# Kernel tuning notes

Measured on AMD Instinct MI355X. Metric: run time of the kernel, lower is better.

## Reference

```python
import jax, jax.numpy as jnp
import numpy as np
import math

NH, NKV, HD = 8, 1, 128
SOFTCAP = 30.0
ROPE_BASE = 500000.0


def _rope_tables(T, hd, base):
    half = hd // 2
    inv_freq = 1.0 / (base ** (np.arange(half, dtype=np.float32) / half))
    t = np.arange(T, dtype=np.float32)
    ang = np.outer(t, inv_freq)  # [T, half]
    return jnp.asarray(np.cos(ang)), jnp.asarray(np.sin(ang))


def apply_rope(x, cos, sin):
    # x: [B, T, H, hd]; cos/sin: [T, hd//2]
    half = x.shape[-1] // 2
    x1, x2 = x[..., :half], x[..., half:]
    T = x.shape[1]
    c = cos[:T][None, :, None, :]
    s = sin[:T][None, :, None, :]
    return jnp.concatenate([x1 * c - x2 * s, x1 * s + x2 * c], axis=-1)


def setup_inputs() -> dict:
    key = jax.random.key(0)
    ks = jax.random.split(key, 5)
    B, T, D = 4, 2048, 1024
    KD = NKV * HD
    x = jax.random.normal(ks[0], (B, T, D), dtype=jnp.float32)
    Wq = jax.random.normal(ks[1], (D, D), dtype=jnp.float32) * (D ** -0.5)
    Wk = jax.random.normal(ks[2], (KD, D), dtype=jnp.float32) * (D ** -0.5)
    Wv = jax.random.normal(ks[3], (KD, D), dtype=jnp.float32) * (D ** -0.5)
    Wo = jax.random.normal(ks[4], (D, D), dtype=jnp.float32) * (D ** -0.5)
    qk_gain = jnp.full((NH,), 1.5, dtype=jnp.float32)  # qk_gain_init
    cos, sin = _rope_tables(T, HD, ROPE_BASE)
    return {"x": x, "Wq": Wq, "Wk": Wk, "Wv": Wv, "Wo": Wo,
            "qk_gain": qk_gain, "cos": cos, "sin": sin}


def reference(x, Wq, Wk, Wv, Wo, qk_gain, cos, sin):
    B, T, D = x.shape
    # projections (QuantLinear with qat disabled == plain linear, no bias)
    q = (x @ Wq.T).reshape(B, T, NH, HD)
    k = (x @ Wk.T).reshape(B, T, NKV, HD)
    v = (x @ Wv.T).reshape(B, T, NKV, HD)
    q = apply_rope(q, cos, sin)
    k = apply_rope(k, cos, sin)
    # learned per-head QK gain applied to queries
    q = q * qk_gain[None, None, :, 1 - 1][..., None] if False else q * qk_gain[None, None, :, None]
    # GQA: broadcast the single kv head across NH query heads
    scale = 1.0 / math.sqrt(HD)
    scores = jnp.einsum('bqhd,bkgd->bhqk', q, k) * scale  # g==NKV==1 broadcast
    # logit softcap before masking/softmax
    scores = SOFTCAP * jnp.tanh(scores / SOFTCAP)
    causal = jnp.tril(jnp.ones((T, T), dtype=bool))
    scores = jnp.where(causal[None, None], scores, -jnp.inf)
    attn = jax.nn.softmax(scores, axis=-1)  # [B, NH, T, T]
    out = jnp.einsum('bhqk,bkgd->bqhd', attn, v).reshape(B, T, NH * HD)
    return out @ Wo.T
```

## Files before the change

### kernel.cpp

```cpp
#include <hip/hip_runtime.h>
#include <hip/hip_bf16.h>

#define B_ 4
#define T_ 2048
#define D_ 1024
#define NH_ 8
#define HD_ 128

typedef short short8 __attribute__((ext_vector_type(8)));
typedef float floatx4 __attribute__((ext_vector_type(4)));

#if __has_builtin(__builtin_amdgcn_exp2f)
#define EXP2F __builtin_amdgcn_exp2f
#else
#define EXP2F exp2f
#endif
#if __has_builtin(__builtin_amdgcn_rcpf)
#define RCPF __builtin_amdgcn_rcpf
#else
__device__ __forceinline__ float RCPF(float x) { return 1.f / x; }
#endif

#if __has_builtin(__builtin_amdgcn_global_load_lds)
#define G2L(gp, lp)                                                        \
  __builtin_amdgcn_global_load_lds(                                        \
      (const __attribute__((address_space(1))) unsigned int*)(gp),         \
      (__attribute__((address_space(3))) unsigned int*)(lp), 16, 0, 0)
#else
#define G2L(gp, lp) (*(uint4*)(lp) = *(const uint4*)(gp))
#endif

__device__ __forceinline__ unsigned short f2b(float f) {
  union { float fl; unsigned int i; } v; v.fl = f;
  unsigned int r = v.i + 0x7fffu + ((v.i >> 16) & 1u);
  return (unsigned short)(r >> 16);
}
__device__ __forceinline__ unsigned int pack_bf16(float a, float b) {
  unsigned int ua = __float_as_uint(a) + 0x8000u;
  unsigned int ub = __float_as_uint(b) + 0x8000u;
  return (ua >> 16) | (ub & 0xffff0000u);
}
__device__ __forceinline__ float blo(unsigned int u) { return __uint_as_float(u << 16); }
__device__ __forceinline__ float bhi(unsigned int u) { return __uint_as_float(u & 0xffff0000u); }

__global__ __launch_bounds__(256) void cvt_kernel(
    const float* __restrict__ x,  const float* __restrict__ wq,
    const float* __restrict__ wk, const float* __restrict__ wv,
    const float* __restrict__ wo, unsigned short* __restrict__ dst)
{
  size_t i = ((size_t)blockIdx.x * 256 + threadIdx.x) * 8;
  const float* src; size_t off;
  if      (i <  8388608u) { src = x;  off = i; }
  else if (i <  9437184u) { src = wq; off = i - 8388608u; }
  else if (i <  9568256u) { src = wk; off = i - 9437184u; }
  else if (i <  9699328u) { src = wv; off = i - 9568256u; }
  else                    { src = wo; off = i - 9699328u; }
  float4 a = *(const float4*)(src + off);
  float4 b = *(const float4*)(src + off + 4);
  uint4 o;
  o.x = pack_bf16(a.x, a.y); o.y = pack_bf16(a.z, a.w);
  o.z = pack_bf16(b.x, b.y); o.w = pack_bf16(b.z, b.w);
  *(uint4*)(dst + i) = o;
}

template <bool C_F32>
__device__ __forceinline__ void gemm_body_1024(
    const unsigned short* __restrict__ Arow0,
    const unsigned short* __restrict__ Btile,
    void* __restrict__ Cb, int ldC)
{
  __shared__ unsigned short As[128 * 32];
  __shared__ unsigned short Bs[128 * 32];
  const int tid = threadIdx.x;
  const int lane = tid & 63;
  const int w = tid >> 6;
  const int wr = w >> 1, wc = w & 1;
  const int l15 = lane & 15, quad = lane >> 4;

  const unsigned short* a_src = Arow0 + (size_t)(tid >> 2) * 1024 + (tid & 3) * 8;
  const unsigned short* b_src = Btile + (size_t)(tid >> 2) * 1024 + (tid & 3) * 8;
  unsigned short* a_dst = &As[(tid >> 2) * 32 + (tid & 3) * 8];
  unsigned short* b_dst = &Bs[(tid >> 2) * 32 + (tid & 3) * 8];

  floatx4 zero = {0.f, 0.f, 0.f, 0.f};
  floatx4 acc[4][4];
#pragma unroll
  for (int i = 0; i < 4; i++)
#pragma unroll
    for (int j = 0; j < 4; j++) acc[i][j] = zero;

  for (int k0 = 0; k0 < 1024; k0 += 32) {
    __syncthreads();
    G2L(a_src + k0,         a_dst);
    G2L(a_src + 65536 + k0, a_dst + 2048);
    G2L(b_src + k0,         b_dst);
    G2L(b_src + 65536 + k0, b_dst + 2048);
    __syncthreads();
    short8 af[4], bfr[4];
#pragma unroll
    for (int i = 0; i < 4; i++)
      af[i] = *(const short8*)&As[(wr * 64 + i * 16 + l15) * 32 + quad * 8];
#pragma unroll
    for (int j = 0; j < 4; j++)
      bfr[j] = *(const short8*)&Bs[(wc * 64 + j * 16 + l15) * 32 + quad * 8];
#pragma unroll
    for (int i = 0; i < 4; i++)
#pragma unroll
      for (int j = 0; j < 4; j++)
        acc[i][j] = __builtin_amdgcn_mfma_f32_16x16x32_bf16(af[i], bfr[j], acc[i][j], 0, 0, 0);
  }
#pragma unroll
  for (int i = 0; i < 4; i++)
#pragma unroll
    for (int j = 0; j < 4; j++)
#pragma unroll
      for (int r = 0; r < 4; r++) {
        size_t off = (size_t)(wr * 64 + i * 16 + quad * 4 + r) * ldC + wc * 64 + j * 16 + l15;
        if (C_F32) ((float*)Cb)[off] = acc[i][j][r];
        else ((unsigned short*)Cb)[off] = f2b(acc[i][j][r]);
      }
}

__global__ __launch_bounds__(256) void gemm_qkv_kernel(
    const unsigned short* __restrict__ x,
    const unsigned short* __restrict__ Wq,
    const unsigned short* __restrict__ Wk,
    const unsigned short* __restrict__ Wv,
    unsigned short* __restrict__ q,
    unsigned short* __restrict__ k,
    unsigned short* __restrict__ v)
{
  const int bx = blockIdx.x, by = blockIdx.y;
  const unsigned short* Btile;
  unsigned short* C;
  int ldC, col0;
  if (by < 8) { Btile = Wq + (size_t)by * 128 * 1024; C = q; ldC = 1024; col0 = by * 128; }
  else if (by == 8) { Btile = Wk; C = k; ldC = 128; col0 = 0; }
  else { Btile = Wv; C = v; ldC = 128; col0 = 0; }
  gemm_body_1024<false>(x + (size_t)bx * 128 * 1024, Btile,
                        C + (size_t)bx * 128 * ldC + col0, ldC);
}

__global__ __launch_bounds__(256) void gemm_out_kernel(
    const unsigned short* __restrict__ ao,
    const unsigned short* __restrict__ Wo,
    float* __restrict__ out)
{
  const int bx = blockIdx.x, by = blockIdx.y;
  gemm_body_1024<true>(ao + (size_t)bx * 128 * 1024, Wo + (size_t)by * 128 * 1024,
                       out + (size_t)bx * 128 * 1024 + by * 128, 1024);
}

__global__ __launch_bounds__(256) void prep_kernel(
    unsigned short* __restrict__ q,
    unsigned short* __restrict__ k,
    const unsigned short* __restrict__ v,
    unsigned short* __restrict__ vT,
    const float* __restrict__ cosT,
    const float* __restrict__ sinT,
    const float* __restrict__ gain)
{
  __shared__ unsigned short tile[32 * 136];
  const int tid = threadIdx.x;
  if (blockIdx.x < 256) {
    const int b = blockIdx.x >> 6, t0 = (blockIdx.x & 63) * 32;
    for (int u = tid; u < 512; u += 256) {
      int r = u >> 4, c = u & 15;
      *(uint4*)&tile[r * 136 + c * 8] =
          *(const uint4*)(v + ((size_t)(b * T_ + t0 + r)) * 128 + c * 8);
    }
    __syncthreads();
    for (int u = tid; u < 512; u += 256) {
      int d = u >> 2, c = u & 3;
      short8 val;
#pragma unroll
      for (int j = 0; j < 8; j++) val[j] = (short)tile[(c * 8 + j) * 136 + d];
      *(short8*)(vT + ((size_t)(b * 128 + d)) * T_ + t0 + c * 8) = val;
    }
    return;
  }
  int idx = (blockIdx.x - 256) * 256 + tid;
  unsigned short* ptr;
  size_t base;
  int t, j;
  float g;
  if (idx < 524288) {
    j = idx & 7;
    int h = (idx >> 3) & 7;
    int bt = idx >> 6;
    t = bt & (T_ - 1);
    base = (size_t)bt * 1024 + h * 128 + j * 8;
    ptr = q;
    g = gain[h] * 0.0029462782549439484f;
  } else {
    int id = idx - 524288;
    j = id & 7;
    int bt = id >> 3;
    t = bt & (T_ - 1);
    base = (size_t)bt * 128 + j * 8;
    ptr = k;
    g = 1.f;
  }
  float4 ca = *(const float4*)&cosT[t * 64 + j * 8];
  float4 cb = *(const float4*)&cosT[t * 64 + j * 8 + 4];
  float4 sa = *(const float4*)&sinT[t * 64 + j * 8];
  float4 sb = *(const float4*)&sinT[t * 64 + j * 8 + 4];
  uint4 lo = *(const uint4*)(ptr + base);
  uint4 hi = *(const uint4*)(ptr + base + 64);
  uint4 olo, ohi;
  {
    float a0 = blo(lo.x), a1 = bhi(lo.x), b0 = blo(hi.x), b1 = bhi(hi.x);
    olo.x = pack_bf16((a0 * ca.x - b0 * sa.x) * g, (a1 * ca.y - b1 * sa.y) * g);
    ohi.x = pack_bf16((a0 * sa.x + b0 * ca.x) * g, (a1 * sa.y + b1 * ca.y) * g);
  }
  {
    float a0 = blo(lo.y), a1 = bhi(lo.y), b0 = blo(hi.y), b1 = bhi(hi.y);
    olo.y = pack_bf16((a0 * ca.z - b0 * sa.z) * g, (a1 * ca.w - b1 * sa.w) * g);
    ohi.y = pack_bf16((a0 * sa.z + b0 * ca.z) * g, (a1 * sa.w + b1 * ca.w) * g);
  }
  {
    float a0 = blo(lo.z), a1 = bhi(lo.z), b0 = blo(hi.z), b1 = bhi(hi.z);
    olo.z = pack_bf16((a0 * cb.x - b0 * sb.x) * g, (a1 * cb.y - b1 * sb.y) * g);
    ohi.z = pack_bf16((a0 * sb.x + b0 * cb.x) * g, (a1 * sb.y + b1 * cb.y) * g);
  }
  {
    float a0 = blo(lo.w), a1 = bhi(lo.w), b0 = blo(hi.w), b1 = bhi(hi.w);
    olo.w = pack_bf16((a0 * cb.z - b0 * sb.z) * g, (a1 * cb.w - b1 * sb.w) * g);
    ohi.w = pack_bf16((a0 * sb.z + b0 * cb.z) * g, (a1 * sb.w + b1 * cb.w) * g);
  }
  *(uint4*)(ptr + base) = olo;
  *(uint4*)(ptr + base + 64) = ohi;
}

template <int NSPLIT>
__global__ __launch_bounds__(256) void attn_kernel(
    const unsigned short* __restrict__ q,
    const unsigned short* __restrict__ k,
    const unsigned short* __restrict__ vT,
    unsigned short* __restrict__ ao,
    unsigned short* __restrict__ Opart,
    float* __restrict__ lbuf)
{
  __shared__ unsigned short Ks[2][16 * 264];
  __shared__ unsigned short Vts[2][128 * 40];

  const int h = blockIdx.y, b = blockIdx.z;
  const int pr   = blockIdx.x / NSPLIT;
  const int part = blockIdx.x % NSPLIT;
  const int tid = threadIdx.x, lane = tid & 63, w = tid >> 6;
  const int l15 = lane & 15, quad = lane >> 4;

  const unsigned short* ksrc =
      k + (size_t)b * T_ * 128 + (size_t)(tid >> 4) * 128 + (tid & 15) * 8;
  const int koff0 = (tid & 15) * 264 + (tid >> 4) * 8;
  const int koff1 = koff0 + 16 * 8;
  const unsigned short* vsrc =
      vT + (size_t)b * 128 * T_ + (size_t)(tid >> 2) * T_ + (tid & 3) * 8;
  const int voff0 = (tid >> 2) * 40 + (tid & 3) * 8;
  const int voff1 = voff0 + 64 * 40;

  const floatx4 zero = {0.f, 0.f, 0.f, 0.f};

  for (int pass = 0; pass < 2; pass++) {
    const int qblock = pass ? (15 - pr) : pr;
    const int qbase = qblock * 128;
    const int qw = qbase + w * 32;
    const int seg = (4 * qblock + 4) / NSPLIT;
    const int ktBeg = part * seg, ktEnd = ktBeg + seg;

    short8 qf[2][4];
#pragma unroll
    for (int g = 0; g < 2; g++) {
      const unsigned short* qrow =
          q + ((size_t)(b * T_ + qw + g * 16 + l15) * NH_ + h) * HD_;
#pragma unroll
      for (int c = 0; c < 4; c++) qf[g][c] = *(const short8*)(qrow + c * 32 + quad * 8);
    }

    float l_i[2] = {0.f, 0.f};
    floatx4 acc[8][2];
#pragma unroll
    for (int d = 0; d < 8; d++) { acc[d][0] = zero; acc[d][1] = zero; }

    __syncthreads();
    {
      uint4 kr0 = *(const uint4*)(ksrc + (size_t)ktBeg * 4096);
      uint4 kr1 = *(const uint4*)(ksrc + (size_t)ktBeg * 4096 + 2048);
      uint4 vr0 = *(const uint4*)(vsrc + ktBeg * 32);
      uint4 vr1 = *(const uint4*)(vsrc + (size_t)64 * T_ + ktBeg * 32);
      unsigned short* kb = Ks[ktBeg & 1];
      unsigned short* vb = Vts[ktBeg & 1];
      *(uint4*)(kb + koff0) = kr0; *(uint4*)(kb + koff1) = kr1;
      *(uint4*)(vb + voff0) = vr0; *(uint4*)(vb + voff1) = vr1;
    }

    for (int kt = ktBeg; kt < ktEnd; kt++) {
      __syncthreads();
      uint4 kr0, kr1, vr0, vr1;
      const bool more = (kt + 1 < ktEnd);
      if (more) {
        kr0 = *(const uint4*)(ksrc + (size_t)(kt + 1) * 4096);
        kr1 = *(const uint4*)(ksrc + (size_t)(kt + 1) * 4096 + 2048);
        vr0 = *(const uint4*)(vsrc + (kt + 1) * 32);
        vr1 = *(const uint4*)(vsrc + (size_t)64 * T_ + (kt + 1) * 32);
      }

      if (kt * 32 <= qw + 31) {
        const unsigned short* KsC = Ks[kt & 1];
        const unsigned short* VtC = Vts[kt & 1];
        floatx4 st[2][2] = {{zero, zero}, {zero, zero}};
#pragma unroll
        for (int c = 0; c < 4; c++) {
          const int dg = (c * 4 + quad) * 264;
          short8 kf0 = *(const short8*)&KsC[dg + l15 * 8];
          short8 kf1 = *(const short8*)&KsC[dg + (16 + l15) * 8];
          st[0][0] = __builtin_amdgcn_mfma_f32_16x16x32_bf16(kf0, qf[0][c], st[0][0], 0, 0, 0);
          st[0][1] = __builtin_amdgcn_mfma_f32_16x16x32_bf16(kf0, qf[1][c], st[0][1], 0, 0, 0);
          st[1][0] = __builtin_amdgcn_mfma_f32_16x16x32_bf16(kf1, qf[0][c], st[1][0], 0, 0, 0);
          st[1][1] = __builtin_amdgcn_mfma_f32_16x16x32_bf16(kf1, qf[1][c], st[1][1], 0, 0, 0);
        }
        float rs[2] = {0.f, 0.f};
        short8 pf0, pf1;
        if (kt * 32 + 31 <= qw) {
#pragma unroll
          for (int g = 0; g < 2; g++) {
            float pv[2][4];
#pragma unroll
            for (int f = 0; f < 2; f++)
#pragma unroll
              for (int r = 0; r < 4; r++) {
                float s = st[f][g][r];
                float e = EXP2F(2.8853901f * s);
                float u = RCPF(e + 1.f);
                float p = EXP2F(-86.561707f * u);
                pv[f][r] = p;
                rs[g] += p;
              }
            unsigned int pa = pack_bf16(pv[0][0], pv[0][1]);
            unsigned int pb = pack_bf16(pv[0][2], pv[0][3]);
            unsigned int pc = pack_bf16(pv[1][0], pv[1][1]);
            unsigned int pd = pack_bf16(pv[1][2], pv[1][3]);
            asm("v_permlane32_swap_b32 %0, %1" : "+v"(pa), "+v"(pc));
            asm("v_permlane32_swap_b32 %0, %1" : "+v"(pb), "+v"(pd));
            asm("v_permlane16_swap_b32 %0, %1" : "+v"(pa), "+v"(pc));
            asm("v_permlane16_swap_b32 %0, %1" : "+v"(pb), "+v"(pd));
            uint4 u; u.x = pa; u.y = pb; u.z = pc; u.w = pd;
            (g ? pf1 : pf0) = *(short8*)&u;
          }
        } else {
#pragma unroll
          for (int g = 0; g < 2; g++) {
            float pv[2][4];
            const int qrow = qw + g * 16 + l15;
#pragma unroll
            for (int f = 0; f < 2; f++)
#pragma unroll
              for (int r = 0; r < 4; r++) {
                float s = st[f][g][r];
                float e = EXP2F(2.8853901f * s);
                float u = RCPF(e + 1.f);
                float p = EXP2F(-86.561707f * u);
                int key = kt * 32 + f * 16 + quad * 4 + r;
                p = (key <= qrow) ? p : 0.f;
                pv[f][r] = p;
                rs[g] += p;
              }
            unsigned int pa = pack_bf16(pv[0][0], pv[0][1]);
            unsigned int pb = pack_bf16(pv[0][2], pv[0][3]);
            unsigned int pc = pack_bf16(pv[1][0], pv[1][1]);
            unsigned int pd = pack_bf16(pv[1][2], pv[1][3]);
            asm("v_permlane32_swap_b32 %0, %1" : "+v"(pa), "+v"(pc));
            asm("v_permlane32_swap_b32 %0, %1" : "+v"(pb), "+v"(pd));
            asm("v_permlane16_swap_b32 %0, %1" : "+v"(pa), "+v"(pc));
            asm("v_permlane16_swap_b32 %0, %1" : "+v"(pb), "+v"(pd));
            uint4 u; u.x = pa; u.y = pb; u.z = pc; u.w = pd;
            (g ? pf1 : pf0) = *(short8*)&u;
          }
        }
#pragma unroll
        for (int g = 0; g < 2; g++) {
          float r2 = rs[g] + __shfl_xor(rs[g], 16);
          l_i[g] += r2 + __shfl_xor(r2, 32);
        }
#pragma unroll
        for (int d = 0; d < 8; d++) {
          short8 vf = *(const short8*)&VtC[(d * 16 + l15) * 40 + quad * 8];
          acc[d][0] = __builtin_amdgcn_mfma_f32_16x16x32_bf16(vf, pf0, acc[d][0], 0, 0, 0);
          acc[d][1] = __builtin_amdgcn_mfma_f32_16x16x32_bf16(vf, pf1, acc[d][1], 0, 0, 0);
        }
      }

      if (more) {
        unsigned short* kb = Ks[(kt + 1) & 1];
        unsigned short* vb = Vts[(kt + 1) & 1];
        *(uint4*)(kb + koff0) = kr0; *(uint4*)(kb + koff1) = kr1;
        *(uint4*)(vb + voff0) = vr0; *(uint4*)(vb + voff1) = vr1;
      }
    }

#pragma unroll
    for (int g = 0; g < 2; g++) {
      const size_t rowidx = (size_t)(b * T_ + qw + g * 16 + l15) * NH_ + h;
      if (NSPLIT == 1) {
        float linv = 1.f / l_i[g];
        unsigned short* aop = ao + rowidx * HD_ + quad * 4;
#pragma unroll
        for (int d = 0; d < 8; d++) {
          uint2 o;
          o.x = pack_bf16(acc[d][g][0] * linv, acc[d][g][1] * linv);
          o.y = pack_bf16(acc[d][g][2] * linv, acc[d][g][3] * linv);
          *(uint2*)(aop + d * 16) = o;
        }
      } else {
        unsigned short* dst =
            ((part == NSPLIT - 1) ? ao : Opart + (size_t)part * 8388608u) +
            rowidx * HD_ + quad * 4;
#pragma unroll
        for (int d = 0; d < 8; d++) {
          uint2 o;
          o.x = pack_bf16(acc[d][g][0], acc[d][g][1]);
          o.y = pack_bf16(acc[d][g][2], acc[d][g][3]);
          *(uint2*)(dst + d * 16) = o;
        }
        if (quad == 0) lbuf[(size_t)part * 65536u + rowidx] = l_i[g];
      }
    }
  }
}

template <int NSPLIT>
__global__ __launch_bounds__(256) void combine_kernel(
    const unsigned short* __restrict__ Opart,
    const float* __restrict__ lbuf,
    unsigned short* __restrict__ ao)
{
  size_t i = ((size_t)blockIdx.x * 256 + threadIdx.x) * 8;
  size_t r = i >> 7;
  float ls = 0.f;
#pragma unroll
  for (int p = 0; p < NSPLIT; p++) ls += lbuf[(size_t)p * 65536u + r];
  float linv = RCPF(ls);
  uint4 c = *(const uint4*)(ao + i);
  float v0 = blo(c.x), v1 = bhi(c.x), v2 = blo(c.y), v3 = bhi(c.y);
  float v4 = blo(c.z), v5 = bhi(c.z), v6 = blo(c.w), v7 = bhi(c.w);
#pragma unroll
  for (int p = 0; p < NSPLIT - 1; p++) {
    uint4 a = *(const uint4*)(Opart + (size_t)p * 8388608u + i);
    v0 += blo(a.x); v1 += bhi(a.x); v2 += blo(a.y); v3 += bhi(a.y);
    v4 += blo(a.z); v5 += bhi(a.z); v6 += blo(a.w); v7 += bhi(a.w);
  }
  uint4 o;
  o.x = pack_bf16(v0 * linv, v1 * linv);
  o.y = pack_bf16(v2 * linv, v3 * linv);
  o.z = pack_bf16(v4 * linv, v5 * linv);
  o.w = pack_bf16(v6 * linv, v7 * linv);
  *(uint4*)(ao + i) = o;
}

extern "C" void kernel_launch(void* const* d_in, const int* in_sizes, int n_in,
                              void* d_out, int out_size, void* d_ws, size_t ws_size,
                              hipStream_t stream) {
  const float* x    = (const float*)d_in[0];
  const float* Wq   = (const float*)d_in[1];
  const float* Wk   = (const float*)d_in[2];
  const float* Wv   = (const float*)d_in[3];
  const float* Wo   = (const float*)d_in[4];
  const float* gain = (const float*)d_in[5];
  const float* cosT = (const float*)d_in[6];
  const float* sinT = (const float*)d_in[7];
  float* out = (float*)d_out;

  unsigned short* ws = (unsigned short*)d_ws;
  unsigned short* blob = ws;
  unsigned short* xb  = blob;
  unsigned short* Wqb = blob + 8388608u;
  unsigned short* Wkb = blob + 9437184u;
  unsigned short* Wvb = blob + 9568256u;
  unsigned short* Wob = blob + 9699328u;
  unsigned short* q   = ws + 10747904u;
  unsigned short* kk  = ws + 19136512u;
  unsigned short* v   = ws + 20185088u;
  unsigned short* vT  = ws + 21233664u;
  unsigned short* ao  = xb;
  unsigned short* Opart = ws + 22282240u;
  float* l2 = (float*)((char*)d_ws + 61341696u);
  const size_t need2 = 61865984ull;
  float* l4 = (float*)((char*)d_ws + 94896128u);
  const size_t need4 = 95944704ull;

  cvt_kernel<<<5248, 256, 0, stream>>>(x, Wq, Wk, Wv, Wo, blob);
  gemm_qkv_kernel<<<dim3(64, 10), 256, 0, stream>>>(xb, Wqb, Wkb, Wvb, q, kk, v);
  prep_kernel<<<2560, 256, 0, stream>>>(q, kk, v, vT, cosT, sinT, gain);
  if (ws_size >= need4) {
    attn_kernel<4><<<dim3(32, 8, 4), 256, 0, stream>>>(q, kk, vT, ao, Opart, l4);
    combine_kernel<4><<<4096, 256, 0, stream>>>(Opart, l4, ao);
  } else if (ws_size >= need2) {
    attn_kernel<2><<<dim3(16, 8, 4), 256, 0, stream>>>(q, kk, vT, ao, Opart, l2);
    combine_kernel<2><<<4096, 256, 0, stream>>>(Opart, l2, ao);
  } else {
    attn_kernel<1><<<dim3(8, 8, 4), 256, 0, stream>>>(q, kk, vT, ao, Opart, l2);
  }
  gemm_out_kernel<<<dim3(64, 8), 256, 0, stream>>>(ao, Wob, out);
}
```

Before: 247.4 us.

## Shrink attention query tile to 16 rows per wave and drop four-way split

Each wave now handles 16 query rows instead of 32, so a block covers 64 rows. This halves the accumulator and score registers, and the launch bounds now request 4 blocks per CU to raise occupancy. The grid is rebalanced: 32 chunk pairs with a 2-way KV split replace the old 4-way split, which cuts combine traffic and partial-output writes. The cost is that each K/V tile loaded into LDS is reused by half as many query rows, so LDS and global traffic per FLOP goes up.

```diff
diff --git a/kernel.cpp b/kernel.cpp
--- a/kernel.cpp
+++ b/kernel.cpp
@@ -233,7 +233,7 @@
 }
 
 template <int NSPLIT>
-__global__ __launch_bounds__(256) void attn_kernel(
+__global__ __launch_bounds__(256, 4) void attn_kernel(
     const unsigned short* __restrict__ q,
     const unsigned short* __restrict__ k,
     const unsigned short* __restrict__ vT,
@@ -262,25 +262,23 @@
   const floatx4 zero = {0.f, 0.f, 0.f, 0.f};
 
   for (int pass = 0; pass < 2; pass++) {
-    const int qblock = pass ? (15 - pr) : pr;
-    const int qbase = qblock * 128;
-    const int qw = qbase + w * 32;
-    const int seg = (4 * qblock + 4) / NSPLIT;
+    const int chunk = pass ? (31 - pr) : pr;
+    const int qw = chunk * 64 + w * 16;
+    const int seg = (2 * chunk + 2) / NSPLIT;
     const int ktBeg = part * seg, ktEnd = ktBeg + seg;
 
-    short8 qf[2][4];
-#pragma unroll
-    for (int g = 0; g < 2; g++) {
+    short8 qf[4];
+    {
       const unsigned short* qrow =
-          q + ((size_t)(b * T_ + qw + g * 16 + l15) * NH_ + h) * HD_;
-#pragma unroll
-      for (int c = 0; c < 4; c++) qf[g][c] = *(const short8*)(qrow + c * 32 + quad * 8);
-    }
-
-    float l_i[2] = {0.f, 0.f};
-    floatx4 acc[8][2];
-#pragma unroll
-    for (int d = 0; d < 8; d++) { acc[d][0] = zero; acc[d][1] = zero; }
+          q + ((size_t)(b * T_ + qw + l15) * NH_ + h) * HD_;
+#pragma unroll
+      for (int c = 0; c < 4; c++) qf[c] = *(const short8*)(qrow + c * 32 + quad * 8);
+    }
+
+    float l_i = 0.f;
+    floatx4 acc[8];
+#pragma unroll
+    for (int d = 0; d < 8; d++) acc[d] = zero;
 
     __syncthreads();
     {
@@ -305,88 +303,69 @@
         vr1 = *(const uint4*)(vsrc + (size_t)64 * T_ + (kt + 1) * 32);
       }
 
-      if (kt * 32 <= qw + 31) {
+      if (kt * 32 <= qw + 15) {
         const unsigned short* KsC = Ks[kt & 1];
         const unsigned short* VtC = Vts[kt & 1];
-        floatx4 st[2][2] = {{zero, zero}, {zero, zero}};
+        floatx4 st[2] = {zero, zero};
 #pragma unroll
         for (int c = 0; c < 4; c++) {
           const int dg = (c * 4 + quad) * 264;
           short8 kf0 = *(const short8*)&KsC[dg + l15 * 8];
           short8 kf1 = *(const short8*)&KsC[dg + (16 + l15) * 8];
-          st[0][0] = __builtin_amdgcn_mfma_f32_16x16x32_bf16(kf0, qf[0][c], st[0][0], 0, 0, 0);
-          st[0][1] = __builtin_amdgcn_mfma_f32_16x16x32_bf16(kf0, qf[1][c], st[0][1], 0, 0, 0);
-          st[1][0] = __builtin_amdgcn_mfma_f32_16x16x32_bf16(kf1, qf[0][c], st[1][0], 0, 0, 0);
-          st[1][1] = __builtin_amdgcn_mfma_f32_16x16x32_bf16(kf1, qf[1][c], st[1][1], 0, 0, 0);
-        }
-        float rs[2] = {0.f, 0.f};
-        short8 pf0, pf1;
-        if (kt * 32 + 31 <= qw) {
-#pragma unroll
-          for (int g = 0; g < 2; g++) {
-            float pv[2][4];
+          st[0] = __builtin_amdgcn_mfma_f32_16x16x32_bf16(kf0, qf[c], st[0], 0, 0, 0);
+          st[1] = __builtin_amdgcn_mfma_f32_16x16x32_bf16(kf1, qf[c], st[1], 0, 0, 0);
+        }
+        float rs = 0.f;
+        short8 pf;
+        {
+          float pv[2][4];
+          if (kt * 32 + 31 <= qw) {
 #pragma unroll
             for (int f = 0; f < 2; f++)
 #pragma unroll
               for (int r = 0; r < 4; r++) {
-                float s = st[f][g][r];
+                float s = st[f][r];
                 float e = EXP2F(2.8853901f * s);
                 float u = RCPF(e + 1.f);
                 float p = EXP2F(-86.561707f * u);
                 pv[f][r] = p;
-                rs[g] += p;
+                rs += p;
               }
-            unsigned int pa = pack_bf16(pv[0][0], pv[0][1]);
-            unsigned int pb = pack_bf16(pv[0][2], pv[0][3]);
-            unsigned int pc = pack_bf16(pv[1][0], pv[1][1]);
-            unsigned int pd = pack_bf16(pv[1][2], pv[1][3]);
-            asm("v_permlane32_swap_b32 %0, %1" : "+v"(pa), "+v"(pc));
-            asm("v_permlane32_swap_b32 %0, %1" : "+v"(pb), "+v"(pd));
-            asm("v_permlane16_swap_b32 %0, %1" : "+v"(pa), "+v"(pc));
-            asm("v_permlane16_swap_b32 %0, %1" : "+v"(pb), "+v"(pd));
-            uint4 u; u.x = pa; u.y = pb; u.z = pc; u.w = pd;
-            (g ? pf1 : pf0) = *(short8*)&u;
-          }
-        } else {
-#pragma unroll
-          for (int g = 0; g < 2; g++) {
-            float pv[2][4];
-            const int qrow = qw + g * 16 + l15;
+          } else {
+            const int qrow = qw + l15;
 #pragma unroll
             for (int f = 0; f < 2; f++)
 #pragma unroll
               for (int r = 0; r < 4; r++) {
-                float s = st[f][g][r];
+                float s = st[f][r];
                 float e = EXP2F(2.8853901f * s);
                 float u = RCPF(e + 1.f);
                 float p = EXP2F(-86.561707f * u);
                 int key = kt * 32 + f * 16 + quad * 4 + r;
                 p = (key <= qrow) ? p : 0.f;
                 pv[f][r] = p;
-                rs[g] += p;
+                rs += p;
               }
-            unsigned int pa = pack_bf16(pv[0][0], pv[0][1]);
-            unsigned int pb = pack_bf16(pv[0][2], pv[0][3]);
-            unsigned int pc = pack_bf16(pv[1][0], pv[1][1]);
-            unsigned int pd = pack_bf16(pv[1][2], pv[1][3]);
-            asm("v_permlane32_swap_b32 %0, %1" : "+v"(pa), "+v"(pc));
-            asm("v_permlane32_swap_b32 %0, %1" : "+v"(pb), "+v"(pd));
-            asm("v_permlane16_swap_b32 %0, %1" : "+v"(pa), "+v"(pc));
-            asm("v_permlane16_swap_b32 %0, %1" : "+v"(pb), "+v"(pd));
-            uint4 u; u.x = pa; u.y = pb; u.z = pc; u.w = pd;
-            (g ? pf1 : pf0) = *(short8*)&u;
           }
-        }
-#pragma unroll
-        for (int g = 0; g < 2; g++) {
-          float r2 = rs[g] + __shfl_xor(rs[g], 16);
-          l_i[g] += r2 + __shfl_xor(r2, 32);
+          unsigned int pa = pack_bf16(pv[0][0], pv[0][1]);
+          unsigned int pb = pack_bf16(pv[0][2], pv[0][3]);
+          unsigned int pc = pack_bf16(pv[1][0], pv[1][1]);
+          unsigned int pd = pack_bf16(pv[1][2], pv[1][3]);
+          asm("v_permlane32_swap_b32 %0, %1" : "+v"(pa), "+v"(pc));
+          asm("v_permlane32_swap_b32 %0, %1" : "+v"(pb), "+v"(pd));
+          asm("v_permlane16_swap_b32 %0, %1" : "+v"(pa), "+v"(pc));
+          asm("v_permlane16_swap_b32 %0, %1" : "+v"(pb), "+v"(pd));
+          uint4 u; u.x = pa; u.y = pb; u.z = pc; u.w = pd;
+          pf = *(short8*)&u;
+        }
+        {
+          float r2 = rs + __shfl_xor(rs, 16);
+          l_i += r2 + __shfl_xor(r2, 32);
         }
 #pragma unroll
         for (int d = 0; d < 8; d++) {
           short8 vf = *(const short8*)&VtC[(d * 16 + l15) * 40 + quad * 8];
-          acc[d][0] = __builtin_amdgcn_mfma_f32_16x16x32_bf16(vf, pf0, acc[d][0], 0, 0, 0);
-          acc[d][1] = __builtin_amdgcn_mfma_f32_16x16x32_bf16(vf, pf1, acc[d][1], 0, 0, 0);
+          acc[d] = __builtin_amdgcn_mfma_f32_16x16x32_bf16(vf, pf, acc[d], 0, 0, 0);
         }
       }
 
@@ -398,17 +377,16 @@
       }
     }
 
-#pragma unroll
-    for (int g = 0; g < 2; g++) {
-      const size_t rowidx = (size_t)(b * T_ + qw + g * 16 + l15) * NH_ + h;
+    {
+      const size_t rowidx = (size_t)(b * T_ + qw + l15) * NH_ + h;
       if (NSPLIT == 1) {
-        float linv = 1.f / l_i[g];
+        float linv = 1.f / l_i;
         unsigned short* aop = ao + rowidx * HD_ + quad * 4;
 #pragma unroll
         for (int d = 0; d < 8; d++) {
           uint2 o;
-          o.x = pack_bf16(acc[d][g][0] * linv, acc[d][g][1] * linv);
-          o.y = pack_bf16(acc[d][g][2] * linv, acc[d][g][3] * linv);
+          o.x = pack_bf16(acc[d][0] * linv, acc[d][1] * linv);
+          o.y = pack_bf16(acc[d][2] * linv, acc[d][3] * linv);
           *(uint2*)(aop + d * 16) = o;
         }
       } else {
@@ -418,11 +396,11 @@
 #pragma unroll
         for (int d = 0; d < 8; d++) {
           uint2 o;
-          o.x = pack_bf16(acc[d][g][0], acc[d][g][1]);
-          o.y = pack_bf16(acc[d][g][2], acc[d][g][3]);
+          o.x = pack_bf16(acc[d][0], acc[d][1]);
+          o.y = pack_bf16(acc[d][2], acc[d][3]);
           *(uint2*)(dst + d * 16) = o;
         }
-        if (quad == 0) lbuf[(size_t)part * 65536u + rowidx] = l_i[g];
+        if (quad == 0) lbuf[(size_t)part * 65536u + rowidx] = l_i;
       }
     }
   }
@@ -485,20 +463,15 @@
   unsigned short* Opart = ws + 22282240u;
   float* l2 = (float*)((char*)d_ws + 61341696u);
   const size_t need2 = 61865984ull;
-  float* l4 = (float*)((char*)d_ws + 94896128u);
-  const size_t need4 = 95944704ull;
 
   cvt_kernel<<<5248, 256, 0, stream>>>(x, Wq, Wk, Wv, Wo, blob);
   gemm_qkv_kernel<<<dim3(64, 10), 256, 0, stream>>>(xb, Wqb, Wkb, Wvb, q, kk, v);
   prep_kernel<<<2560, 256, 0, stream>>>(q, kk, v, vT, cosT, sinT, gain);
-  if (ws_size >= need4) {
-    attn_kernel<4><<<dim3(32, 8, 4), 256, 0, stream>>>(q, kk, vT, ao, Opart, l4);
-    combine_kernel<4><<<4096, 256, 0, stream>>>(Opart, l4, ao);
-  } else if (ws_size >= need2) {
-    attn_kernel<2><<<dim3(16, 8, 4), 256, 0, stream>>>(q, kk, vT, ao, Opart, l2);
+  if (ws_size >= need2) {
+    attn_kernel<2><<<dim3(32, 8, 4), 256, 0, stream>>>(q, kk, vT, ao, Opart, l2);
     combine_kernel<2><<<4096, 256, 0, stream>>>(Opart, l2, ao);
   } else {
-    attn_kernel<1><<<dim3(8, 8, 4), 256, 0, stream>>>(q, kk, vT, ao, Opart, l2);
+    attn_kernel<1><<<dim3(16, 8, 4), 256, 0, stream>>>(q, kk, vT, ao, Opart, l2);
   }
   gemm_out_kernel<<<dim3(64, 8), 256, 0, stream>>>(ao, Wob, out);
 }
```

Measured after the change: 234.3 us. 5.3% less time.
